# Kernel tuning notes

Hardware: AMD Instinct MI355X
Metric: run time of the kernel (lower is better)

Reference implementation:

```python
import jax, jax.numpy as jnp
import numpy as np

N, E, DIN, H, C = 50000, 800000, 256, 4, 32  # nodes, edges, in_dim, heads, per-head dim
NEG_SLOPE = 0.2  # PyG GATConv default LeakyReLU slope


def setup_inputs() -> dict:
    key = jax.random.key(0)
    ks = jax.random.split(key, 12)
    x = jax.random.normal(ks[0], (N, DIN), jnp.float32)
    edge_index = jax.random.randint(ks[1], (2, E), 0, N, dtype=jnp.int64)
    # layer 1: in=DIN -> heads*C; layer 2: in=H*C -> heads*C (concat=True default)
    W1 = jax.random.normal(ks[2], (DIN, H * C), jnp.float32) / np.sqrt(DIN).astype(np.float32)
    as1 = jax.random.normal(ks[3], (H, C), jnp.float32) * 0.1
    ad1 = jax.random.normal(ks[4], (H, C), jnp.float32) * 0.1
    b1 = jnp.zeros((H * C,), jnp.float32)
    W2 = jax.random.normal(ks[5], (H * C, H * C), jnp.float32) / np.sqrt(H * C).astype(np.float32)
    as2 = jax.random.normal(ks[6], (H, C), jnp.float32) * 0.1
    ad2 = jax.random.normal(ks[7], (H, C), jnp.float32) * 0.1
    b2 = jnp.zeros((H * C,), jnp.float32)
    return {"x": x, "edge_index": edge_index, "W1": W1, "as1": as1, "ad1": ad1,
            "b1": b1, "W2": W2, "as2": as2, "ad2": ad2, "b2": b2}


def gat_conv(x, src, dst, W, a_src, a_dst, b):
    # x: [N, Fin] -> h: [N, H, C]
    n = x.shape[0]
    h = (x @ W).reshape(n, H, C)
    # per-node attention logits [N, H]
    e_src = jnp.einsum('nhc,hc->nh', h, a_src)
    e_dst = jnp.einsum('nhc,hc->nh', h, a_dst)
    # edge-wise logits + segment softmax over destination neighborhoods
    e = jax.nn.leaky_relu(e_src[src] + e_dst[dst], NEG_SLOPE)  # [Et, H]
    m = jax.ops.segment_max(e, dst, num_segments=n)
    ex = jnp.exp(e - m[dst])
    s = jax.ops.segment_sum(ex, dst, num_segments=n)
    alpha = ex / s[dst]  # self-loops guarantee every node has >=1 edge
    # weighted scatter-add aggregation
    out = jax.ops.segment_sum(h[src] * alpha[:, :, None], dst, num_segments=n)
    return out.reshape(n, H * C) + b


def reference(x, edge_index, W1, as1, ad1, b1, W2, as2, ad2, b2):
    n = x.shape[0]
    loop = jnp.arange(n, dtype=edge_index.dtype)
    src = jnp.concatenate([edge_index[0], loop])  # PyG GATConv adds self-loops
    dst = jnp.concatenate([edge_index[1], loop])
    h = jax.nn.elu(gat_conv(x, src, dst, W1, as1, ad1, b1))
    # dropout is a no-op in eval mode (F.dropout with training=False)
    out = jax.nn.elu(gat_conv(h, src, dst, W2, as2, ad2, b2))
    return out
```

## Files before the change

### kernel.cpp

```cpp
#include <hip/hip_runtime.h>
#include <hip/hip_fp16.h>
#include <type_traits>

#define NN 50000
#define NE 800000
#define ET (NE + NN)
#define NEG 0.2f
#define GGRID 782
#define EGRID 3321

typedef __attribute__((ext_vector_type(4))) float f32x4;
typedef __attribute__((ext_vector_type(8))) short s16x8;

#define GLD_LDS16(g, l)                                                        \
  __builtin_amdgcn_global_load_lds(                                            \
      (const __attribute__((address_space(1))) void*)(g),                      \
      (__attribute__((address_space(3))) void*)(l), 16, 0, 0)

__device__ __forceinline__ float lrelu(float x) { return x > 0.0f ? x : NEG * x; }
__device__ __forceinline__ float elu1(float x) { return x > 0.0f ? x : __expf(x) - 1.0f; }
__device__ __forceinline__ unsigned short f2bf(float f) {
  unsigned u = __float_as_uint(f);
  u += 0x7FFFu + ((u >> 16) & 1u);
  return (unsigned short)(u >> 16);
}
__device__ __forceinline__ float bf2f(unsigned short h) {
  return __uint_as_float(((unsigned)h) << 16);
}

__global__ void wprep_kernel(const float* __restrict__ W1, short* __restrict__ W1h,
                             short* __restrict__ W1l, const float* __restrict__ W2,
                             short* __restrict__ W2h, short* __restrict__ W2l,
                             int* __restrict__ cnt) {
  int gid = blockIdx.x * 256 + threadIdx.x;
  for (int i = gid; i < NN; i += 192 * 256) cnt[i] = 0;
  int idx = gid;
  const float* W; short* Wth; short* Wtl; int Kdim;
  if (idx < 256 * 128) { W = W1; Wth = W1h; Wtl = W1l; Kdim = 256; }
  else {
    idx -= 256 * 128;
    W = W2; Wth = W2h; Wtl = W2l; Kdim = 128;
  }
  int k = idx >> 7, n = idx & 127;
  float w = W[idx];
  unsigned short h = f2bf(w);
  unsigned short l = f2bf(w - bf2f(h));
  Wth[n * Kdim + k] = (short)h;
  Wtl[n * Kdim + k] = (short)l;
}

template<int K, typename AT, bool CSR>
__global__ __launch_bounds__(256) void gemm_mfma(const AT* __restrict__ A,
                                                 const short* __restrict__ Bth,
                                                 const short* __restrict__ Btl,
                                                 const float* __restrict__ a_s,
                                                 const float* __restrict__ a_d,
                                                 __half* __restrict__ outh,
                                                 float* __restrict__ es,
                                                 float* __restrict__ ed,
                                                 const int* __restrict__ ei,
                                                 int* __restrict__ cnt,
                                                 int* __restrict__ colw) {
  int bid = blockIdx.x;
  if constexpr (CSR) {
    if (bid < EGRID) {
      int e = bid * 256 + threadIdx.x;
      if (e < ET) {
        int src, dst;
        if (e < NE) { src = ei[e]; dst = ei[NE + e]; } else { src = dst = e - NE; }
        int r = atomicAdd(&cnt[dst], 1);
        if (r < 128) colw[(dst << 7) + r] = src;
      }
      return;
    }
    bid -= EGRID;
  }
  constexpr int NSTEP = K / 32;
  __shared__ short Ah[64 * 32], Al[64 * 32];
  __shared__ short Bh[128 * 32], Bl[128 * 32];
  const int tid = threadIdx.x;
  const int lane = tid & 63;
  const int wv = tid >> 6;
  const int wm = wv >> 1, wn = wv & 1;
  const int row0 = bid * 64;
  const int srow = tid >> 2;
  const int skc = tid & 3;

  f32x4 acc[2][4];
#pragma unroll
  for (int i = 0; i < 2; ++i)
#pragma unroll
    for (int j = 0; j < 4; ++j) acc[i][j] = (f32x4){0.f, 0.f, 0.f, 0.f};

  for (int s = 0; s < NSTEP; ++s) {
    __syncthreads();
    {
      int grow = row0 + srow; grow = grow < NN ? grow : NN - 1;
      const AT* ap = &A[(size_t)grow * K + s * 32 + skc * 8];
      float xs[8];
      if constexpr (std::is_same_v<AT, float>) {
        float4 x0 = *(const float4*)ap;
        float4 x1 = *(const float4*)(ap + 4);
        xs[0]=x0.x; xs[1]=x0.y; xs[2]=x0.z; xs[3]=x0.w;
        xs[4]=x1.x; xs[5]=x1.y; xs[6]=x1.z; xs[7]=x1.w;
      } else {
        int4 raw = *(const int4*)ap;
        const __half2* hv = (const __half2*)&raw;
#pragma unroll
        for (int q = 0; q < 4; ++q) {
          float2 f = __half22float2(hv[q]);
          xs[2 * q] = f.x; xs[2 * q + 1] = f.y;
        }
      }
      int hi[4], lo[4];
#pragma unroll
      for (int q = 0; q < 4; ++q) {
        unsigned short h0 = f2bf(xs[2 * q]);
        unsigned short l0 = f2bf(xs[2 * q] - bf2f(h0));
        unsigned short h1 = f2bf(xs[2 * q + 1]);
        unsigned short l1 = f2bf(xs[2 * q + 1] - bf2f(h1));
        hi[q] = (int)(((unsigned)h1 << 16) | h0);
        lo[q] = (int)(((unsigned)l1 << 16) | l0);
      }
      *(int4*)&Ah[srow * 32 + skc * 8] = make_int4(hi[0], hi[1], hi[2], hi[3]);
      *(int4*)&Al[srow * 32 + skc * 8] = make_int4(lo[0], lo[1], lo[2], lo[3]);
    }
#pragma unroll
    for (int rr = 0; rr < 2; ++rr) {
      int n = srow + rr * 64;
      const short* gh = &Bth[(size_t)n * K + s * 32 + skc * 8];
      const short* gl = &Btl[(size_t)n * K + s * 32 + skc * 8];
      char* lbh = (char*)Bh + rr * 4096 + wv * 1024;
      char* lbl = (char*)Bl + rr * 4096 + wv * 1024;
      GLD_LDS16(gh, lbh);
      GLD_LDS16(gl, lbl);
    }
    __syncthreads();
    const int fr = lane & 15;
    const int fk = (lane >> 4) * 8;
    s16x8 ah[2], al[2], bh[4], bl[4];
#pragma unroll
    for (int mf = 0; mf < 2; ++mf) {
      int r = wm * 32 + mf * 16 + fr;
      ah[mf] = *(const s16x8*)&Ah[r * 32 + fk];
      al[mf] = *(const s16x8*)&Al[r * 32 + fk];
    }
#pragma unroll
    for (int nf = 0; nf < 4; ++nf) {
      int n = wn * 64 + nf * 16 + fr;
      bh[nf] = *(const s16x8*)&Bh[n * 32 + fk];
      bl[nf] = *(const s16x8*)&Bl[n * 32 + fk];
    }
#pragma unroll
    for (int mf = 0; mf < 2; ++mf)
#pragma unroll
      for (int nf = 0; nf < 4; ++nf) {
        acc[mf][nf] = __builtin_amdgcn_mfma_f32_16x16x32_bf16(ah[mf], bh[nf], acc[mf][nf], 0, 0, 0);
        acc[mf][nf] = __builtin_amdgcn_mfma_f32_16x16x32_bf16(ah[mf], bl[nf], acc[mf][nf], 0, 0, 0);
        acc[mf][nf] = __builtin_amdgcn_mfma_f32_16x16x32_bf16(al[mf], bh[nf], acc[mf][nf], 0, 0, 0);
      }
  }

  const int fr = lane & 15;
  const int fg = lane >> 4;
  float asr[4], adr[4];
#pragma unroll
  for (int nf = 0; nf < 4; ++nf) {
    int c = wn * 64 + nf * 16 + fr;
    asr[nf] = a_s[c]; adr[nf] = a_d[c];
  }
#pragma unroll
  for (int mf = 0; mf < 2; ++mf) {
#pragma unroll
    for (int r = 0; r < 4; ++r) {
      int row = row0 + wm * 32 + mf * 16 + fg * 4 + r;
      float sp0 = acc[mf][0][r] * asr[0] + acc[mf][1][r] * asr[1];
      float sp1 = acc[mf][2][r] * asr[2] + acc[mf][3][r] * asr[3];
      float dp0 = acc[mf][0][r] * adr[0] + acc[mf][1][r] * adr[1];
      float dp1 = acc[mf][2][r] * adr[2] + acc[mf][3][r] * adr[3];
#pragma unroll
      for (int off = 1; off < 16; off <<= 1) {
        sp0 += __shfl_xor(sp0, off); sp1 += __shfl_xor(sp1, off);
        dp0 += __shfl_xor(dp0, off); dp1 += __shfl_xor(dp1, off);
      }
      if (row < NN) {
#pragma unroll
        for (int nf = 0; nf < 4; ++nf)
          outh[(size_t)row * 128 + wn * 64 + nf * 16 + fr] = __float2half(acc[mf][nf][r]);
        if (fr == 0) {
          es[row * 4 + wn * 2 + 0] = sp0;
          es[row * 4 + wn * 2 + 1] = sp1;
          ed[row * 4 + wn * 2 + 0] = dp0;
          ed[row * 4 + wn * 2 + 1] = dp1;
        }
      }
    }
  }
}

template<typename OT>
__global__ __launch_bounds__(128) void agg_fused(const __half* __restrict__ h,
                                                 const float4* __restrict__ es4,
                                                 const float4* __restrict__ ed4,
                                                 const int* __restrict__ cnt,
                                                 const int* __restrict__ col,
                                                 const float* __restrict__ bias,
                                                 OT* __restrict__ out) {
  __shared__ float wc[2][512];
  __shared__ int   cc[2][128];
  int wid = (blockIdx.x * 128 + threadIdx.x) >> 6;
  if (wid >= NN) return;
  const int lane = threadIdx.x & 63;
  const int wv = (threadIdx.x >> 6) & 1;
  int deg = cnt[wid];
  deg = deg < 128 ? deg : 128;
  const int start = wid << 7;
  const float4 edv = ed4[wid];
  const char* hb = (const char*)h;

  const bool v0 = lane < deg, v1 = lane + 64 < deg;
  int c0 = 0, c1 = 0;
  float4 e0, e1;
  if (v0) { c0 = col[start + lane]; e0 = es4[c0]; }
  if (v1) { c1 = col[start + lane + 64]; e1 = es4[c1]; }
  float s0 = 0.f, s1 = 0.f, s2 = 0.f, s3 = 0.f;
  float4 p0, p1;
  if (v0) {
    p0.x = __expf(lrelu(e0.x + edv.x)); p0.y = __expf(lrelu(e0.y + edv.y));
    p0.z = __expf(lrelu(e0.z + edv.z)); p0.w = __expf(lrelu(e0.w + edv.w));
    s0 += p0.x; s1 += p0.y; s2 += p0.z; s3 += p0.w;
  }
  if (v1) {
    p1.x = __expf(lrelu(e1.x + edv.x)); p1.y = __expf(lrelu(e1.y + edv.y));
    p1.z = __expf(lrelu(e1.z + edv.z)); p1.w = __expf(lrelu(e1.w + edv.w));
    s0 += p1.x; s1 += p1.y; s2 += p1.z; s3 += p1.w;
  }
#pragma unroll
  for (int off = 32; off; off >>= 1) {
    s0 += __shfl_xor(s0, off); s1 += __shfl_xor(s1, off);
    s2 += __shfl_xor(s2, off); s3 += __shfl_xor(s3, off);
  }
  const float i0 = 1.0f / s0, i1 = 1.0f / s1, i2 = 1.0f / s2, i3 = 1.0f / s3;
  if (v0) {
    float4 w; w.x = p0.x * i0; w.y = p0.y * i1; w.z = p0.z * i2; w.w = p0.w * i3;
    *(float4*)&wc[wv][lane * 4] = w;
    cc[wv][lane] = c0 << 8;
  }
  if (v1) {
    float4 w; w.x = p1.x * i0; w.y = p1.y * i1; w.z = p1.z * i2; w.w = p1.w * i3;
    *(float4*)&wc[wv][(lane + 64) * 4] = w;
    cc[wv][lane + 64] = c1 << 8;
  }
  if (lane == 0 && (deg & 1)) {
    cc[wv][deg] = cc[wv][0];
    float4 z = {0.f, 0.f, 0.f, 0.f};
    *(float4*)&wc[wv][deg * 4] = z;
  }

  const int half_ = lane >> 5;
  const int fl = lane & 31;
  const int hd2 = fl >> 3;
  const int fb = fl << 3;
  float a0 = 0.f, a1 = 0.f, a2 = 0.f, a3 = 0.f;
  const int degR = (deg + 1) & ~1;
  int jj = 0;
  for (; jj + 8 <= degR; jj += 8) {
    int off[4]; float w[4];
#pragma unroll
    for (int u = 0; u < 4; ++u) {
      int e = jj + 2 * u + half_;
      off[u] = cc[wv][e];
      w[u] = wc[wv][e * 4 + hd2];
    }
    int2 q[4];
#pragma unroll
    for (int u = 0; u < 4; ++u) q[u] = *(const int2*)(hb + off[u] + fb);
#pragma unroll
    for (int u = 0; u < 4; ++u) {
      float2 f0 = __half22float2(*(const __half2*)&q[u].x);
      float2 f1 = __half22float2(*(const __half2*)&q[u].y);
      a0 = fmaf(f0.x, w[u], a0); a1 = fmaf(f0.y, w[u], a1);
      a2 = fmaf(f1.x, w[u], a2); a3 = fmaf(f1.y, w[u], a3);
    }
  }
  for (; jj < degR; jj += 2) {
    int e = jj + half_;
    int off = cc[wv][e];
    float w = wc[wv][e * 4 + hd2];
    int2 q = *(const int2*)(hb + off + fb);
    float2 f0 = __half22float2(*(const __half2*)&q.x);
    float2 f1 = __half22float2(*(const __half2*)&q.y);
    a0 = fmaf(f0.x, w, a0); a1 = fmaf(f0.y, w, a1);
    a2 = fmaf(f1.x, w, a2); a3 = fmaf(f1.y, w, a3);
  }
  a0 += __shfl_xor(a0, 32); a1 += __shfl_xor(a1, 32);
  a2 += __shfl_xor(a2, 32); a3 += __shfl_xor(a3, 32);

  float4 bs = *(const float4*)&bias[fl * 4];
  if (half_ == 0) {
    float o0 = elu1(a0 + bs.x), o1 = elu1(a1 + bs.y);
    float o2 = elu1(a2 + bs.z), o3 = elu1(a3 + bs.w);
    if constexpr (std::is_same_v<OT, float>) {
      float4 o; o.x = o0; o.y = o1; o.z = o2; o.w = o3;
      *(float4*)&out[(size_t)wid * 128 + fl * 4] = o;
    } else {
      __half2 h01 = __floats2half2_rn(o0, o1);
      __half2 h23 = __floats2half2_rn(o2, o3);
      int2 pk; pk.x = *(int*)&h01; pk.y = *(int*)&h23;
      *(int2*)&out[(size_t)wid * 128 + fl * 4] = pk;
    }
  }
}

extern "C" void kernel_launch(void* const* d_in, const int* in_sizes, int n_in,
                              void* d_out, int out_size, void* d_ws, size_t ws_size,
                              hipStream_t stream) {
  const float* x   = (const float*)d_in[0];
  const int*   ei  = (const int*)d_in[1];
  const float* W1  = (const float*)d_in[2];
  const float* as1 = (const float*)d_in[3];
  const float* ad1 = (const float*)d_in[4];
  const float* b1  = (const float*)d_in[5];
  const float* W2  = (const float*)d_in[6];
  const float* as2 = (const float*)d_in[7];
  const float* ad2 = (const float*)d_in[8];
  const float* b2  = (const float*)d_in[9];

  char* ws = (char*)d_ws;
  __half* h     = (__half*)(ws);
  float*  es    = (float*) (ws + 12800000);
  float*  ed    = (float*) (ws + 13600000);
  int*    cnt   = (int*)   (ws + 14400000);
  int*    col   = (int*)   (ws + 14600064);
  short*  wt1h  = (short*) (ws + 40200064);
  short*  wt1l  = (short*) (ws + 40265600);
  short*  wt2h  = (short*) (ws + 40331136);
  short*  wt2l  = (short*) (ws + 40363904);
  __half* h2    = (__half*)d_out;

  wprep_kernel<<<192, 256, 0, stream>>>(W1, wt1h, wt1l, W2, wt2h, wt2l, cnt);

  int ngrid = (NN + 1) / 2;

  gemm_mfma<256, float, true><<<EGRID + GGRID, 256, 0, stream>>>(
      x, wt1h, wt1l, as1, ad1, h, es, ed, ei, cnt, col);

  agg_fused<__half><<<ngrid, 128, 0, stream>>>(h, (const float4*)es, (const float4*)ed,
                                               cnt, col, b1, h2);

  gemm_mfma<128, __half, false><<<GGRID, 256, 0, stream>>>(
      h2, wt2h, wt2l, as2, ad2, h, es, ed, nullptr, nullptr, nullptr);

  agg_fused<float><<<ngrid, 128, 0, stream>>>(h, (const float4*)es, (const float4*)ed,
                                              cnt, col, b2, (float*)d_out);
}
```

Baseline: 185.6 us.

## Move edge-count atomics into prep kernel and scatter columns using precomputed ranks

Per-destination atomic counting moves out of the first GEMM launch into the weight-prep kernel, which writes each edge's rank to a new buffer. The GEMM launch then only scatters src indices to colw using the stored rank, and its GEMM blocks now come before the edge blocks in the grid. Counter zeroing becomes a separate hipMemsetAsync. This aims to take atomic contention off the GEMM's critical path, at the cost of an extra rank array write/read, a larger edge-index read, and one more stream operation.

```diff
diff --git a/kernel.cpp b/kernel.cpp
--- a/kernel.cpp
+++ b/kernel.cpp
@@ -28,13 +28,19 @@
   return __uint_as_float(((unsigned)h) << 16);
 }
 
-__global__ void wprep_kernel(const float* __restrict__ W1, short* __restrict__ W1h,
-                             short* __restrict__ W1l, const float* __restrict__ W2,
-                             short* __restrict__ W2h, short* __restrict__ W2l,
-                             int* __restrict__ cnt) {
-  int gid = blockIdx.x * 256 + threadIdx.x;
-  for (int i = gid; i < NN; i += 192 * 256) cnt[i] = 0;
-  int idx = gid;
+__global__ void prep_count_kernel(const float* __restrict__ W1, short* __restrict__ W1h,
+                                  short* __restrict__ W1l, const float* __restrict__ W2,
+                                  short* __restrict__ W2h, short* __restrict__ W2l,
+                                  const int* __restrict__ ei, int* __restrict__ cnt,
+                                  int* __restrict__ rank) {
+  if (blockIdx.x >= 192) {
+    int e = (blockIdx.x - 192) * 256 + threadIdx.x;
+    if (e >= ET) return;
+    int dst = (e < NE) ? ei[NE + e] : (e - NE);
+    rank[e] = atomicAdd(&cnt[dst], 1);
+    return;
+  }
+  int idx = blockIdx.x * 256 + threadIdx.x;
   const float* W; short* Wth; short* Wtl; int Kdim;
   if (idx < 256 * 128) { W = W1; Wth = W1h; Wtl = W1l; Kdim = 256; }
   else {
@@ -59,21 +65,19 @@
                                                  float* __restrict__ es,
                                                  float* __restrict__ ed,
                                                  const int* __restrict__ ei,
-                                                 int* __restrict__ cnt,
+                                                 const int* __restrict__ rank,
                                                  int* __restrict__ colw) {
-  int bid = blockIdx.x;
   if constexpr (CSR) {
-    if (bid < EGRID) {
-      int e = bid * 256 + threadIdx.x;
+    if (blockIdx.x >= GGRID) {
+      int e = (blockIdx.x - GGRID) * 256 + threadIdx.x;
       if (e < ET) {
         int src, dst;
         if (e < NE) { src = ei[e]; dst = ei[NE + e]; } else { src = dst = e - NE; }
-        int r = atomicAdd(&cnt[dst], 1);
+        int r = rank[e];
         if (r < 128) colw[(dst << 7) + r] = src;
       }
       return;
     }
-    bid -= EGRID;
   }
   constexpr int NSTEP = K / 32;
   __shared__ short Ah[64 * 32], Al[64 * 32];
@@ -82,7 +86,7 @@
   const int lane = tid & 63;
   const int wv = tid >> 6;
   const int wm = wv >> 1, wn = wv & 1;
-  const int row0 = bid * 64;
+  const int row0 = blockIdx.x * 64;
   const int srow = tid >> 2;
   const int skc = tid & 3;
 
@@ -332,18 +336,22 @@
   float*  ed    = (float*) (ws + 13600000);
   int*    cnt   = (int*)   (ws + 14400000);
   int*    col   = (int*)   (ws + 14600064);
-  short*  wt1h  = (short*) (ws + 40200064);
-  short*  wt1l  = (short*) (ws + 40265600);
-  short*  wt2h  = (short*) (ws + 40331136);
-  short*  wt2l  = (short*) (ws + 40363904);
+  int*    rank  = (int*)   (ws + 40200064);
+  short*  wt1h  = (short*) (ws + 43600064);
+  short*  wt1l  = (short*) (ws + 43665600);
+  short*  wt2h  = (short*) (ws + 43731136);
+  short*  wt2l  = (short*) (ws + 43763904);
   __half* h2    = (__half*)d_out;
 
-  wprep_kernel<<<192, 256, 0, stream>>>(W1, wt1h, wt1l, W2, wt2h, wt2l, cnt);
+  hipMemsetAsync(cnt, 0, NN * sizeof(int), stream);
+
+  prep_count_kernel<<<192 + EGRID, 256, 0, stream>>>(W1, wt1h, wt1l, W2, wt2h, wt2l,
+                                                     ei, cnt, rank);
 
   int ngrid = (NN + 1) / 2;
 
-  gemm_mfma<256, float, true><<<EGRID + GGRID, 256, 0, stream>>>(
-      x, wt1h, wt1l, as1, ad1, h, es, ed, ei, cnt, col);
+  gemm_mfma<256, float, true><<<GGRID + EGRID, 256, 0, stream>>>(
+      x, wt1h, wt1l, as1, ad1, h, es, ed, ei, rank, col);
 
   agg_fused<__half><<<ngrid, 128, 0, stream>>>(h, (const float4*)es, (const float4*)ed,
                                                cnt, col, b1, h2);
```

After: 166.0 us (median of 2 runs). 10.6% less time.
